# Kernel tuning notes

Hardware: AMD Instinct MI355X
Metric: run time of the kernel (lower is better)

The kernel has to match this reference:

```python
import math
import jax, jax.numpy as jnp
import numpy as np

B, T, C = 4, 2048, 1024
H = 16
HS = C // H  # head_size = 64

def setup_inputs() -> dict:
    key = jax.random.key(0)
    k1, k2, k3 = jax.random.split(key, 3)
    x = jax.random.normal(k1, (B, T, C), dtype=jnp.float32)
    W_qkv = jax.random.normal(k2, (C, 3 * C), dtype=jnp.float32) * (1.0 / math.sqrt(C))
    W_proj = jax.random.normal(k3, (C, C), dtype=jnp.float32) * (1.0 / math.sqrt(C))
    b_proj = jnp.zeros((C,), dtype=jnp.float32)
    return {"x": x, "W_qkv": W_qkv, "W_proj": W_proj, "b_proj": b_proj}

def reference(x, W_qkv, W_proj, b_proj):
    Bx, Tx, Cx = x.shape
    qkv = x @ W_qkv  # [B,T,3C]
    q, k, v = jnp.split(qkv, 3, axis=-1)
    # [B,T,C] -> [B,H,T,HS]
    def heads(t):
        return t.reshape(Bx, Tx, H, HS).transpose(0, 2, 1, 3)
    q, k, v = heads(q), heads(k), heads(v)
    scores = jnp.einsum('bhqd,bhkd->bhqk', q, k) / math.sqrt(HS)
    causal = jnp.tril(jnp.ones((Tx, Tx), dtype=bool))
    scores = jnp.where(causal, scores, -jnp.inf)
    attn = jax.nn.softmax(scores, axis=-1)
    out = jnp.einsum('bhqk,bhkd->bhqd', attn, v)  # [B,H,T,HS]
    out = out.transpose(0, 2, 1, 3).reshape(Bx, Tx, Cx)
    return out @ W_proj + b_proj
```

## Files before the change

kernel.cpp:

```cpp
#include <hip/hip_runtime.h>
#include <hip/hip_bf16.h>
#include <cstdint>
#include <cstddef>

using bf16 = __hip_bfloat16;
typedef __attribute__((ext_vector_type(8))) short short8;
typedef __attribute__((ext_vector_type(4))) float floatx4;

#define B_ 4
#define T_ 2048
#define C_ 1024
#define H_ 16
#define HS_ 64
#define BT_ (B_*T_)
#define N3C (3*C_)

#define MFMA16(a,b,c) __builtin_amdgcn_mfma_f32_16x16x32_bf16((a),(b),(c),0,0,0)

#if __has_builtin(__builtin_amdgcn_exp2f)
#define EXP2(x) __builtin_amdgcn_exp2f(x)
#else
#define EXP2(x) exp2f(x)
#endif

static __device__ __forceinline__ void gld16(const bf16* g, bf16* l) {
  __builtin_amdgcn_global_load_lds(
      (const __attribute__((address_space(1))) unsigned int*)g,
      (__attribute__((address_space(3))) unsigned int*)l, 16, 0, 0);
}

static __device__ __forceinline__ unsigned short f2bf_us(float x) {
  bf16 b = __float2bfloat16(x);
  return *(unsigned short*)&b;
}

__global__ __launch_bounds__(256)
void k_prep(const float* __restrict__ x, bf16* __restrict__ xb,
            const float* __restrict__ Wqkv, bf16* __restrict__ wqkvT,
            const float* __restrict__ Wproj, bf16* __restrict__ wprojT)
{
  const int bid = blockIdx.x, tid = threadIdx.x;
  __shared__ float tile[64][65];

  if (bid < 4096) {
    const int i = bid*256 + tid;
    const float4 v0 = ((const float4*)x)[2*i];
    const float4 v1 = ((const float4*)x)[2*i + 1];
    union { bf16 b[8]; uint4 u; } cvt;
    cvt.b[0] = __float2bfloat16(v0.x);
    cvt.b[1] = __float2bfloat16(v0.y);
    cvt.b[2] = __float2bfloat16(v0.z);
    cvt.b[3] = __float2bfloat16(v0.w);
    cvt.b[4] = __float2bfloat16(v1.x);
    cvt.b[5] = __float2bfloat16(v1.y);
    cvt.b[6] = __float2bfloat16(v1.z);
    cvt.b[7] = __float2bfloat16(v1.w);
    ((uint4*)xb)[i] = cvt.u;
    return;
  }

  const float* in; bf16* out; int N, n0, k0;
  if (bid < 4864) {
    const int j = bid - 4096;
    in = Wqkv; out = wqkvT; N = N3C;
    n0 = (j % 48) * 64; k0 = (j / 48) * 64;
  } else {
    const int j = bid - 4864;
    in = Wproj; out = wprojT; N = C_;
    n0 = (j % 16) * 64; k0 = (j / 16) * 64;
  }
  const int r = tid >> 6, c = tid & 63;
  #pragma unroll
  for (int j = 0; j < 16; ++j)
    tile[r + j*4][c] = in[(size_t)(k0 + r + j*4) * N + n0 + c];
  __syncthreads();
  #pragma unroll
  for (int j = 0; j < 16; ++j) {
    int rr = r + j*4;
    out[(size_t)(n0 + rr) * C_ + k0 + c] = __float2bfloat16(tile[c][rr]);
  }
}

template<int MODE, int NB>
__global__ __launch_bounds__(256, 2)
void k_gemm(const bf16* __restrict__ A, const bf16* __restrict__ Bt,
            int N, int K,
            bf16* __restrict__ Qb, bf16* __restrict__ Kb, bf16* __restrict__ Vt,
            float* __restrict__ Out, const float* __restrict__ bias)
{
  __shared__ __align__(16) char smem[65536];
  bf16* const sA = (bf16*)smem;
  bf16* const sB = (bf16*)(smem + 32768);

  const int tid  = threadIdx.x;
  const int lane = tid & 63, wave = tid >> 6;
  const int quad = lane >> 4, l16 = lane & 15;
  const int wm = wave >> 1, wn = wave & 1;

  const int g = blockIdx.x;
  const int xcd = g & 7;
  const int local = g >> 3;
  const int nb = local % NB;
  const int mb = (local / NB) * 8 + xcd;
  const int m0 = mb * 128, n0 = nb * 128;

  const int ra = tid >> 2;
  const int gc = (tid & 3) ^ ((ra >> 1) & 3);
  const bf16* aptr = A  + (size_t)(m0 + ra) * K + gc*8;
  const bf16* bptr = Bt + (size_t)(n0 + ra) * K + gc*8;
  const size_t rj = (size_t)64 * K;

  const int KT = K >> 5;
  floatx4 acc[4][4] = {};
  const int swz = (l16 >> 1) & 3;
  const int aoff = (wm*64 + l16)*32 + (quad ^ swz)*8;
  const int boff = (wn*64 + l16)*32 + (quad ^ swz)*8;

  #pragma unroll
  for (int t = 0; t < 3; ++t) {
    bf16* sa = sA + t*4096; bf16* sb = sB + t*4096;
    gld16(aptr + t*32,      sa + tid*8);
    gld16(aptr + rj + t*32, sa + 2048 + tid*8);
    gld16(bptr + t*32,      sb + tid*8);
    gld16(bptr + rj + t*32, sb + 2048 + tid*8);
  }

  #pragma unroll 1
  for (int i = 0; i < KT; ++i) {
    if (i < KT-2)       asm volatile("s_waitcnt vmcnt(8)" ::: "memory");
    else if (i == KT-2) asm volatile("s_waitcnt vmcnt(4)" ::: "memory");
    else                asm volatile("s_waitcnt vmcnt(0)" ::: "memory");
    asm volatile("s_barrier" ::: "memory");
    if (i < KT-3) {
      const int t = i + 3;
      bf16* sa = sA + (t & 3)*4096; bf16* sb = sB + (t & 3)*4096;
      gld16(aptr + t*32,      sa + tid*8);
      gld16(aptr + rj + t*32, sa + 2048 + tid*8);
      gld16(bptr + t*32,      sb + tid*8);
      gld16(bptr + rj + t*32, sb + 2048 + tid*8);
    }
    const bf16* sa = sA + (i & 3)*4096;
    const bf16* sb = sB + (i & 3)*4096;
    short8 af[4], bfm[4];
    #pragma unroll
    for (int ii = 0; ii < 4; ++ii) af[ii]  = *(const short8*)&sa[aoff + ii*512];
    #pragma unroll
    for (int j = 0; j < 4; ++j)    bfm[j]  = *(const short8*)&sb[boff + j*512];
    __builtin_amdgcn_s_setprio(1);
    #pragma unroll
    for (int ii = 0; ii < 4; ++ii)
      #pragma unroll
      for (int j = 0; j < 4; ++j)
        acc[ii][j] = MFMA16(af[ii], bfm[j], acc[ii][j]);
    __builtin_amdgcn_s_setprio(0);
  }

  if (MODE == 0 && nb >= 16) {
    __syncthreads();
    unsigned short* epi = (unsigned short*)smem;
    #pragma unroll
    for (int i = 0; i < 4; ++i) {
      const int tl = wm*64 + i*16 + quad*4;
      #pragma unroll
      for (int j = 0; j < 4; ++j) {
        const int ccl = wn*64 + j*16 + l16;
        #pragma unroll
        for (int r = 0; r < 4; ++r)
          epi[ccl*132 + tl + r] = f2bf_us(acc[i][j][r]);
      }
    }
    __syncthreads();
    const int b  = m0 >> 11;
    const int t0 = m0 & 2047;
    const int h0 = (n0 - 2*C_) >> 6;
    #pragma unroll
    for (int it = 0; it < 32; ++it) {
      const int id = it*256 + tid;
      const int tp = id & 31;
      const int rest = id >> 5;
      const int tl64 = (rest & 1) * 64;
      const int ccl = rest >> 1;
      const int k0p = tp + (tp & 16);
      const unsigned lo = epi[ccl*132 + tl64 + k0p];
      const unsigned hi = epi[ccl*132 + tl64 + k0p + 16];
      const int h = h0 + (ccl >> 6), d = ccl & 63;
      unsigned* row = (unsigned*)(Vt + ((size_t)(b*H_ + h) * HS_ + d) * T_);
      row[(t0 >> 1) + tl64/2 + tp] = lo | (hi << 16);
    }
  } else {
    #pragma unroll
    for (int i = 0; i < 4; ++i) {
      const int rowb = m0 + wm*64 + i*16 + quad*4;
      #pragma unroll
      for (int j = 0; j < 4; ++j) {
        const int col = n0 + wn*64 + j*16 + l16;
        #pragma unroll
        for (int r = 0; r < 4; ++r) {
          const float v = acc[i][j][r];
          const int rr = rowb + r;
          if (MODE == 0) {
            const int b = rr >> 11, t = rr & 2047;
            const int h = (col >> 6) & 15, d = col & 63;
            const size_t addr = (((size_t)(b*H_ + h) * T_ + t) << 6) + d;
            if (nb < 8) {
              Qb[addr] = __float2bfloat16(v * 0.18033688f);
            } else {
              Kb[addr] = __float2bfloat16(v);
            }
          } else {
            Out[(size_t)rr * N + col] = v + bias[col];
          }
        }
      }
    }
  }
}

__global__ __launch_bounds__(256, 3)
void k_attn(const bf16* __restrict__ Q, const bf16* __restrict__ K,
            const bf16* __restrict__ Vt, bf16* __restrict__ att)
{
  __shared__ bf16 kbuf[2][64*64];
  __shared__ bf16 vbuf[2][64*64];
  __shared__ bf16 pbuf[4][32*64];

  const int tid  = threadIdx.x;
  const int lane = tid & 63, wave = tid >> 6;
  const int quad = lane >> 4, l16 = lane & 15;
  const int x7 = l16 & 7;

  const int g  = blockIdx.x;
  const int bh = (g & 7) * 8 + ((g >> 3) & 7);
  const int qt = 15 - (g >> 6);
  const int b = bh >> 4, h = bh & 15;

  const bf16* Qp = Q  + (size_t)bh * T_ * HS_;
  const bf16* Kp = K  + (size_t)bh * T_ * HS_;
  const bf16* Vp = Vt + (size_t)bh * HS_ * T_;

  const int qbase = qt*128 + wave*32;
  const int ntk = 2*qt + 2;

  short8 qf[2][2];
  #pragma unroll
  for (int mt = 0; mt < 2; ++mt)
    #pragma unroll
    for (int ss = 0; ss < 2; ++ss)
      qf[mt][ss] = *(const short8*)(Qp + (size_t)(qbase + mt*16 + l16) * HS_ + ss*32 + quad*8);

  floatx4 o[2][4] = {};
  float lrow[2][4] = {};

  const bf16* kg[2]; const bf16* vg[2];
  int ldsoff[2];
  #pragma unroll
  for (int it = 0; it < 2; ++it) {
    const int c = it*256 + tid;
    const int row = c >> 3;
    const int col = (c & 7) ^ (row & 7);
    kg[it] = Kp + (size_t)row * HS_ + col*8;
    vg[it] = Vp + (size_t)row * T_ + col*8;
    ldsoff[it] = c*8;
  }

  bf16* pw = pbuf[wave];
  unsigned int* pw32 = (unsigned int*)pw;
  const int c0 = l16 >> 2;
  const int dwl = l16 & 3;

  for (int i = 0; i <= ntk; ++i) {
    __syncthreads();
    if (i < ntk) {
      const int stk0 = i * 64;
      bf16* kb = kbuf[i & 1];
      bf16* vb = vbuf[i & 1];
      #pragma unroll
      for (int it = 0; it < 2; ++it) {
        gld16(kg[it] + (size_t)stk0 * HS_, kb + ldsoff[it]);
        gld16(vg[it] + stk0,               vb + ldsoff[it]);
      }
    }
    if (i == 0) continue;
    const int tk  = i - 1;
    const int tk0 = tk * 64;
    if (tk0 > qbase + 31) continue;
    const bf16* kb = kbuf[tk & 1];
    const bf16* vb = vbuf[tk & 1];

    floatx4 s[2][4] = {};
    __builtin_amdgcn_s_setprio(1);
    #pragma unroll
    for (int nt = 0; nt < 4; ++nt) {
      const int key = nt*16 + l16;
      #pragma unroll
      for (int ss = 0; ss < 2; ++ss) {
        short8 kf = *(const short8*)&kb[(key*8 + ((ss*4+quad) ^ x7))*8];
        s[0][nt] = MFMA16(qf[0][ss], kf, s[0][nt]);
        s[1][nt] = MFMA16(qf[1][ss], kf, s[1][nt]);
      }
    }
    __builtin_amdgcn_s_setprio(0);

    if (tk0 + 63 > qbase) {
      #pragma unroll
      for (int mt = 0; mt < 2; ++mt)
        #pragma unroll
        for (int nt = 0; nt < 4; ++nt) {
          const int key = tk0 + nt*16 + l16;
          #pragma unroll
          for (int r = 0; r < 4; ++r) {
            const int qr = qbase + mt*16 + quad*4 + r;
            if (key > qr) s[mt][nt][r] = -1e30f;
          }
        }
    }

    #pragma unroll
    for (int mt = 0; mt < 2; ++mt) {
      #pragma unroll
      for (int r = 0; r < 4; ++r) {
        const float p0 = EXP2(s[mt][0][r]), p1 = EXP2(s[mt][1][r]);
        const float p2 = EXP2(s[mt][2][r]), p3 = EXP2(s[mt][3][r]);
        lrow[mt][r] += (p0 + p1) + (p2 + p3);
        const int q = mt*16 + quad*4 + r;
        const unsigned w0 = __builtin_amdgcn_perm(__float_as_uint(p1), __float_as_uint(p0), 0x07060302u);
        const unsigned w1 = __builtin_amdgcn_perm(__float_as_uint(p3), __float_as_uint(p2), 0x07060302u);
        pw32[q*32 + (((c0 + q)     & 7) << 2) + dwl] = w0;
        pw32[q*32 + (((c0 + q + 4) & 7) << 2) + dwl] = w1;
      }
    }

    __builtin_amdgcn_s_setprio(1);
    #pragma unroll
    for (int ss = 0; ss < 2; ++ss) {
      short8 pf0 = *(const short8*)&pw[l16*64      + ((4*ss + quad + l16) & 7)*8];
      short8 pf1 = *(const short8*)&pw[(16+l16)*64 + ((4*ss + quad + l16) & 7)*8];
      #pragma unroll
      for (int nd = 0; nd < 4; ++nd) {
        const int d = nd*16 + l16;
        short8 vf = *(const short8*)&vb[(d*8 + ((ss*4+quad) ^ x7))*8];
        o[0][nd] = MFMA16(pf0, vf, o[0][nd]);
        o[1][nd] = MFMA16(pf1, vf, o[1][nd]);
      }
    }
    __builtin_amdgcn_s_setprio(0);
  }

  #pragma unroll
  for (int mt = 0; mt < 2; ++mt) {
    #pragma unroll
    for (int r = 0; r < 4; ++r) {
      float lsum = lrow[mt][r];
      lsum += __shfl_xor(lsum, 1);
      lsum += __shfl_xor(lsum, 2);
      lsum += __shfl_xor(lsum, 4);
      lsum += __shfl_xor(lsum, 8);
      const float inv = 1.0f / lsum;
      const int tt = qbase + mt*16 + quad*4 + r;
      #pragma unroll
      for (int nd = 0; nd < 4; ++nd)
        att[(size_t)(b*T_ + tt) * C_ + h*64 + nd*16 + l16] =
            __float2bfloat16(o[mt][nd][r] * inv);
    }
  }
}

extern "C" void kernel_launch(void* const* d_in, const int* in_sizes, int n_in,
                              void* d_out, int out_size, void* d_ws, size_t ws_size,
                              hipStream_t stream) {
  const float* x     = (const float*)d_in[0];
  const float* Wqkv  = (const float*)d_in[1];
  const float* Wproj = (const float*)d_in[2];
  const float* bproj = (const float*)d_in[3];
  float* out = (float*)d_out;

  char* ws = (char*)d_ws;
  bf16* xb     = (bf16*)(ws + 0);
  bf16* wqkvT  = (bf16*)(ws + 16777216);
  bf16* wprojT = (bf16*)(ws + 23068672);
  bf16* Qb     = (bf16*)(ws + 25165824);
  bf16* Kb     = (bf16*)(ws + 41943040);
  bf16* Vt     = (bf16*)(ws + 58720256);
  bf16* att    = (bf16*)(ws + 75497472);

  k_prep<<<dim3(5120), 256, 0, stream>>>(x, xb, Wqkv, wqkvT, Wproj, wprojT);
  k_gemm<0, 24><<<dim3(1536), 256, 0, stream>>>(
      xb, wqkvT, N3C, C_, Qb, Kb, Vt, nullptr, nullptr);
  k_attn<<<dim3(1024), 256, 0, stream>>>(Qb, Kb, Vt, att);
  k_gemm<1, 8><<<dim3(512), 256, 0, stream>>>(
      att, wprojT, C_, C_, nullptr, nullptr, nullptr, out, bproj);
}
```

Before: 226.7 us.

## Use double-buffered BK=64 pipeline for QKV GEMM, keep old pipeline in projection kernel

The QKV GEMM drops its 4-stage BK=32 pipeline, which used manual vmcnt waits, in favour of a simpler double-buffered BK=64 loop. That loop uses an 8-way XOR LDS swizzle and a __syncthreads per iteration. The previous pipelined GEMM is copied into a separate k_proj kernel for the output projection, with a direct fp32 epilogue. This looks like an experiment to see whether fewer, larger k-steps beat deeper prefetch. The cost is less latency hiding, since there is only one tile in flight, plus full barriers in the QKV GEMM.

After: 225.5 us. Within noise of the previous version (-0.5%).

```diff
diff --git a/kernel.cpp b/kernel.cpp
--- a/kernel.cpp
+++ b/kernel.cpp
@@ -89,8 +89,8 @@
             float* __restrict__ Out, const float* __restrict__ bias)
 {
   __shared__ __align__(16) char smem[65536];
-  bf16* const sA = (bf16*)smem;
-  bf16* const sB = (bf16*)(smem + 32768);
+  bf16* const sAb = (bf16*)smem;
+  bf16* const sBb = (bf16*)(smem + 32768);
 
   const int tid  = threadIdx.x;
   const int lane = tid & 63, wave = tid >> 6;
@@ -104,55 +104,46 @@
   const int mb = (local / NB) * 8 + xcd;
   const int m0 = mb * 128, n0 = nb * 128;
 
-  const int ra = tid >> 2;
-  const int gc = (tid & 3) ^ ((ra >> 1) & 3);
+  const int ra = tid >> 3;
+  const int gc = (tid & 7) ^ (ra & 7);
   const bf16* aptr = A  + (size_t)(m0 + ra) * K + gc*8;
   const bf16* bptr = Bt + (size_t)(n0 + ra) * K + gc*8;
-  const size_t rj = (size_t)64 * K;
-
-  const int KT = K >> 5;
+  const size_t rj = (size_t)32 * K;
+
   floatx4 acc[4][4] = {};
-  const int swz = (l16 >> 1) & 3;
-  const int aoff = (wm*64 + l16)*32 + (quad ^ swz)*8;
-  const int boff = (wn*64 + l16)*32 + (quad ^ swz)*8;
-
-  #pragma unroll
-  for (int t = 0; t < 3; ++t) {
-    bf16* sa = sA + t*4096; bf16* sb = sB + t*4096;
-    gld16(aptr + t*32,      sa + tid*8);
-    gld16(aptr + rj + t*32, sa + 2048 + tid*8);
-    gld16(bptr + t*32,      sb + tid*8);
-    gld16(bptr + rj + t*32, sb + 2048 + tid*8);
-  }
-
-  #pragma unroll 1
-  for (int i = 0; i < KT; ++i) {
-    if (i < KT-2)       asm volatile("s_waitcnt vmcnt(8)" ::: "memory");
-    else if (i == KT-2) asm volatile("s_waitcnt vmcnt(4)" ::: "memory");
-    else                asm volatile("s_waitcnt vmcnt(0)" ::: "memory");
-    asm volatile("s_barrier" ::: "memory");
-    if (i < KT-3) {
-      const int t = i + 3;
-      bf16* sa = sA + (t & 3)*4096; bf16* sb = sB + (t & 3)*4096;
-      gld16(aptr + t*32,      sa + tid*8);
-      gld16(aptr + rj + t*32, sa + 2048 + tid*8);
-      gld16(bptr + t*32,      sb + tid*8);
-      gld16(bptr + rj + t*32, sb + 2048 + tid*8);
-    }
-    const bf16* sa = sA + (i & 3)*4096;
-    const bf16* sb = sB + (i & 3)*4096;
-    short8 af[4], bfm[4];
-    #pragma unroll
-    for (int ii = 0; ii < 4; ++ii) af[ii]  = *(const short8*)&sa[aoff + ii*512];
-    #pragma unroll
-    for (int j = 0; j < 4; ++j)    bfm[j]  = *(const short8*)&sb[boff + j*512];
-    __builtin_amdgcn_s_setprio(1);
-    #pragma unroll
-    for (int ii = 0; ii < 4; ++ii)
-      #pragma unroll
-      for (int j = 0; j < 4; ++j)
-        acc[ii][j] = MFMA16(af[ii], bfm[j], acc[ii][j]);
-    __builtin_amdgcn_s_setprio(0);
+  const int KI = K >> 6;
+  const int x7a = l16 & 7;
+
+  for (int i = 0; i <= KI; ++i) {
+    __syncthreads();
+    if (i < KI) {
+      const int k0 = i << 6;
+      bf16* sa = sAb + (i & 1) * 8192;
+      bf16* sb = sBb + (i & 1) * 8192;
+      #pragma unroll
+      for (int q2 = 0; q2 < 4; ++q2) {
+        gld16(aptr + q2*rj + k0, sa + q2*2048 + tid*8);
+        gld16(bptr + q2*rj + k0, sb + q2*2048 + tid*8);
+      }
+    }
+    if (i == 0) continue;
+    const bf16* sa = sAb + ((i-1) & 1) * 8192;
+    const bf16* sb = sBb + ((i-1) & 1) * 8192;
+    #pragma unroll
+    for (int ks = 0; ks < 2; ++ks) {
+      short8 af[4], bfm[4];
+      #pragma unroll
+      for (int ii = 0; ii < 4; ++ii)
+        af[ii] = *(const short8*)&sa[(wm*64 + ii*16 + l16)*64 + ((ks*4 + quad) ^ x7a)*8];
+      #pragma unroll
+      for (int ii = 0; ii < 4; ++ii)
+        bfm[ii] = *(const short8*)&sb[(wn*64 + ii*16 + l16)*64 + ((ks*4 + quad) ^ x7a)*8];
+      #pragma unroll
+      for (int ii = 0; ii < 4; ++ii)
+        #pragma unroll
+        for (int j = 0; j < 4; ++j)
+          acc[ii][j] = MFMA16(af[ii], bfm[j], acc[ii][j]);
+    }
   }
 
   if (MODE == 0 && nb >= 16) {
@@ -216,6 +207,91 @@
   }
 }
 
+template<int NB>
+__global__ __launch_bounds__(256, 2)
+void k_proj(const bf16* __restrict__ A, const bf16* __restrict__ Bt,
+            int N, int K, float* __restrict__ Out, const float* __restrict__ bias)
+{
+  __shared__ __align__(16) char smem[65536];
+  bf16* const sA = (bf16*)smem;
+  bf16* const sB = (bf16*)(smem + 32768);
+
+  const int tid  = threadIdx.x;
+  const int lane = tid & 63, wave = tid >> 6;
+  const int quad = lane >> 4, l16 = lane & 15;
+  const int wm = wave >> 1, wn = wave & 1;
+
+  const int g = blockIdx.x;
+  const int xcd = g & 7;
+  const int local = g >> 3;
+  const int nb = local % NB;
+  const int mb = (local / NB) * 8 + xcd;
+  const int m0 = mb * 128, n0 = nb * 128;
+
+  const int ra = tid >> 2;
+  const int gc = (tid & 3) ^ ((ra >> 1) & 3);
+  const bf16* aptr = A  + (size_t)(m0 + ra) * K + gc*8;
+  const bf16* bptr = Bt + (size_t)(n0 + ra) * K + gc*8;
+  const size_t rj = (size_t)64 * K;
+
+  const int KT = K >> 5;
+  floatx4 acc[4][4] = {};
+  const int swz = (l16 >> 1) & 3;
+  const int aoff = (wm*64 + l16)*32 + (quad ^ swz)*8;
+  const int boff = (wn*64 + l16)*32 + (quad ^ swz)*8;
+
+  #pragma unroll
+  for (int t = 0; t < 3; ++t) {
+    bf16* sa = sA + t*4096; bf16* sb = sB + t*4096;
+    gld16(aptr + t*32,      sa + tid*8);
+    gld16(aptr + rj + t*32, sa + 2048 + tid*8);
+    gld16(bptr + t*32,      sb + tid*8);
+    gld16(bptr + rj + t*32, sb + 2048 + tid*8);
+  }
+
+  #pragma unroll 1
+  for (int i = 0; i < KT; ++i) {
+    if (i < KT-2)       asm volatile("s_waitcnt vmcnt(8)" ::: "memory");
+    else if (i == KT-2) asm volatile("s_waitcnt vmcnt(4)" ::: "memory");
+    else                asm volatile("s_waitcnt vmcnt(0)" ::: "memory");
+    asm volatile("s_barrier" ::: "memory");
+    if (i < KT-3) {
+      const int t = i + 3;
+      bf16* sa = sA + (t & 3)*4096; bf16* sb = sB + (t & 3)*4096;
+      gld16(aptr + t*32,      sa + tid*8);
+      gld16(aptr + rj + t*32, sa + 2048 + tid*8);
+      gld16(bptr + t*32,      sb + tid*8);
+      gld16(bptr + rj + t*32, sb + 2048 + tid*8);
+    }
+    const bf16* sa = sA + (i & 3)*4096;
+    const bf16* sb = sB + (i & 3)*4096;
+    short8 af[4], bfm[4];
+    #pragma unroll
+    for (int ii = 0; ii < 4; ++ii) af[ii]  = *(const short8*)&sa[aoff + ii*512];
+    #pragma unroll
+    for (int j = 0; j < 4; ++j)    bfm[j]  = *(const short8*)&sb[boff + j*512];
+    __builtin_amdgcn_s_setprio(1);
+    #pragma unroll
+    for (int ii = 0; ii < 4; ++ii)
+      #pragma unroll
+      for (int j = 0; j < 4; ++j)
+        acc[ii][j] = MFMA16(af[ii], bfm[j], acc[ii][j]);
+    __builtin_amdgcn_s_setprio(0);
+  }
+
+  #pragma unroll
+  for (int i = 0; i < 4; ++i) {
+    const int rowb = m0 + wm*64 + i*16 + quad*4;
+    #pragma unroll
+    for (int j = 0; j < 4; ++j) {
+      const int col = n0 + wn*64 + j*16 + l16;
+      #pragma unroll
+      for (int r = 0; r < 4; ++r)
+        Out[(size_t)(rowb + r) * N + col] = acc[i][j][r] + bias[col];
+    }
+  }
+}
+
 __global__ __launch_bounds__(256, 3)
 void k_attn(const bf16* __restrict__ Q, const bf16* __restrict__ K,
             const bf16* __restrict__ Vt, bf16* __restrict__ att)
@@ -387,6 +463,6 @@
   k_gemm<0, 24><<<dim3(1536), 256, 0, stream>>>(
       xb, wqkvT, N3C, C_, Qb, Kb, Vt, nullptr, nullptr);
   k_attn<<<dim3(1024), 256, 0, stream>>>(Qb, Kb, Vt, att);
-  k_gemm<1, 8><<<dim3(512), 256, 0, stream>>>(
-      att, wprojT, C_, C_, nullptr, nullptr, nullptr, out, bproj);
-}
+  k_proj<8><<<dim3(512), 256, 0, stream>>>(
+      att, wprojT, C_, C_, out, bproj);
+}
```

## Add dedicated large-tile QKV GEMM kernel with 3-stage pipeline and 8 waves

Applied to the files above, without the earlier changes.

Replaces the generic QKV GEMM, which used 128x128 tiles and 1536 blocks, with a specialized kernel. Each 512-thread block computes a 256x384 tile covering matching Q, K and V column slices of one head pair, over a triple-buffered LDS pipeline that splits loads and MFMAs into half-steps with explicit barriers. The intent is more operand reuse per LDS load and better load/compute overlap. The cost is 120KB of LDS with one block per CU, only 256 blocks for the whole device, and high register pressure from 48 accumulators. The projection GEMM is split into its own simplified kernel.

Result: faster. 217.6 us (-4.0%).

```diff
diff --git a/kernel.cpp b/kernel.cpp
--- a/kernel.cpp
+++ b/kernel.cpp
@@ -81,12 +81,158 @@
   }
 }
 
-template<int MODE, int NB>
+__global__ __launch_bounds__(512, 1)
+void k_gemmqkv(const bf16* __restrict__ A, const bf16* __restrict__ Bt,
+               bf16* __restrict__ Qb, bf16* __restrict__ Kb, bf16* __restrict__ Vt)
+{
+  __shared__ __align__(16) char smem[122880];
+  bf16* const sA = (bf16*)smem;
+  bf16* const sB = (bf16*)(smem + 49152);
+
+  const int tid  = threadIdx.x;
+  const int lane = tid & 63, wave = tid >> 6;
+  const int quad = lane >> 4, l16 = lane & 15;
+  const int wm = wave >> 2, wn = wave & 3;
+
+  const int g = blockIdx.x;
+  const int xcd = g & 7;
+  const int local = g >> 3;
+  const int nb = local & 7;
+  const int mb = (local >> 3) * 8 + xcd;
+  const int m0 = mb * 256;
+  const int n0q = nb * 128;
+
+  const int ra = tid >> 2;
+  const int gc = (tid & 3) ^ ((ra >> 1) & 3);
+  const bf16* aptr = A  + (size_t)(m0 + ra) * C_ + gc*8;
+  const bf16* bp0  = Bt + (size_t)(n0q + ra) * C_ + gc*8;
+  const bf16* bp1  = Bt + (size_t)(1024 + n0q + ra) * C_ + gc*8;
+  const bf16* bp2  = Bt + (size_t)(2048 + n0q + ra) * C_ + gc*8;
+
+  floatx4 acc[8][6] = {};
+  const int swz = (l16 >> 1) & 3;
+  const int aoff = (wm*128 + l16)*32 + (quad ^ swz)*8;
+  const int boff = (wn*96  + l16)*32 + (quad ^ swz)*8;
+
+#define STAGE_A(t,s) { bf16* d = sA + (s)*8192;                     \
+    gld16(aptr + (t)*32,                  d + tid*8);               \
+    gld16(aptr + (size_t)128*C_ + (t)*32, d + 4096 + tid*8); }
+#define STAGE_B(t,s) { bf16* d = sB + (s)*12288;                    \
+    gld16(bp0 + (t)*32, d + tid*8);                                 \
+    gld16(bp1 + (t)*32, d + 4096 + tid*8);                          \
+    gld16(bp2 + (t)*32, d + 8192 + tid*8); }
+
+  STAGE_A(0,0); STAGE_B(0,0);
+  STAGE_A(1,1); STAGE_B(1,1);
+  asm volatile("s_waitcnt vmcnt(5)" ::: "memory");
+  asm volatile("s_barrier" ::: "memory");
+
+  int cs = 0;
+  #pragma unroll 1
+  for (int i = 0; i < 32; ++i) {
+    const int s2 = (cs >= 1) ? cs - 1 : 2;
+    const bf16* sa = sA + cs*8192;
+    const bf16* sb = sB + cs*12288;
+    short8 bq[6], af[4];
+    #pragma unroll
+    for (int j = 0; j < 6; ++j)    bq[j]  = *(const short8*)&sb[boff + j*512];
+    #pragma unroll
+    for (int ii = 0; ii < 4; ++ii) af[ii] = *(const short8*)&sa[aoff + ii*512];
+    if (i < 30) STAGE_A(i+2, s2);
+    asm volatile("s_barrier" ::: "memory");
+    asm volatile("s_waitcnt lgkmcnt(0)" ::: "memory");
+    __builtin_amdgcn_sched_barrier(0);
+    __builtin_amdgcn_s_setprio(1);
+    #pragma unroll
+    for (int ii = 0; ii < 4; ++ii)
+      #pragma unroll
+      for (int j = 0; j < 6; ++j)
+        acc[ii][j] = MFMA16(af[ii], bq[j], acc[ii][j]);
+    __builtin_amdgcn_s_setprio(0);
+    asm volatile("s_barrier" ::: "memory");
+    #pragma unroll
+    for (int ii = 0; ii < 4; ++ii) af[ii] = *(const short8*)&sa[aoff + (4+ii)*512];
+    if (i < 30) {
+      STAGE_B(i+2, s2);
+      asm volatile("s_waitcnt vmcnt(5)" ::: "memory");
+    } else if (i == 30) {
+      asm volatile("s_waitcnt vmcnt(0)" ::: "memory");
+    }
+    asm volatile("s_barrier" ::: "memory");
+    asm volatile("s_waitcnt lgkmcnt(0)" ::: "memory");
+    __builtin_amdgcn_sched_barrier(0);
+    __builtin_amdgcn_s_setprio(1);
+    #pragma unroll
+    for (int ii = 0; ii < 4; ++ii)
+      #pragma unroll
+      for (int j = 0; j < 6; ++j)
+        acc[4+ii][j] = MFMA16(af[ii], bq[j], acc[4+ii][j]);
+    __builtin_amdgcn_s_setprio(0);
+    asm volatile("s_barrier" ::: "memory");
+    cs = (cs == 2) ? 0 : cs + 1;
+  }
+#undef STAGE_A
+#undef STAGE_B
+
+  #pragma unroll
+  for (int ii = 0; ii < 8; ++ii) {
+    const int rowb = m0 + wm*128 + ii*16 + quad*4;
+    #pragma unroll
+    for (int j = 0; j < 6; ++j) {
+      const int L = wn*96 + j*16 + l16;
+      if (L < 256) {
+        const int gcol = (L < 128) ? (n0q + L) : (1024 + n0q + L - 128);
+        const int h = (gcol >> 6) & 15, d = gcol & 63;
+        #pragma unroll
+        for (int r = 0; r < 4; ++r) {
+          const int rr = rowb + r;
+          const int b = rr >> 11, t = rr & 2047;
+          const size_t addr = (((size_t)(b*H_ + h) * T_ + t) << 6) + d;
+          if (L < 128) Qb[addr] = __float2bfloat16(acc[ii][j][r] * 0.18033688f);
+          else         Kb[addr] = __float2bfloat16(acc[ii][j][r]);
+        }
+      }
+    }
+  }
+
+  unsigned short* epi = (unsigned short*)smem;
+  #pragma unroll
+  for (int ii = 0; ii < 8; ++ii) {
+    const int tl = wm*128 + ii*16 + quad*4;
+    #pragma unroll
+    for (int j = 0; j < 6; ++j) {
+      const int L = wn*96 + j*16 + l16;
+      if (L >= 256) {
+        const int ccl = L - 256;
+        #pragma unroll
+        for (int r = 0; r < 4; ++r)
+          epi[ccl*258 + tl + r] = f2bf_us(acc[ii][j][r]);
+      }
+    }
+  }
+  __syncthreads();
+  const int b  = m0 >> 11;
+  const int t0 = m0 & 2047;
+  #pragma unroll
+  for (int it = 0; it < 32; ++it) {
+    const int id = it*512 + tid;
+    const int tp = id & 31;
+    const int rest = id >> 5;
+    const int tl64 = (rest & 3) * 64;
+    const int ccl = rest >> 2;
+    const int k0p = tp + (tp & 16);
+    const unsigned lo = epi[ccl*258 + tl64 + k0p];
+    const unsigned hi = epi[ccl*258 + tl64 + k0p + 16];
+    const int h = nb*2 + (ccl >> 6), d = ccl & 63;
+    unsigned* row = (unsigned*)(Vt + ((size_t)(b*H_ + h) * HS_ + d) * T_);
+    row[(t0 >> 1) + tl64/2 + tp] = lo | (hi << 16);
+  }
+}
+
+template<int NB>
 __global__ __launch_bounds__(256, 2)
-void k_gemm(const bf16* __restrict__ A, const bf16* __restrict__ Bt,
-            int N, int K,
-            bf16* __restrict__ Qb, bf16* __restrict__ Kb, bf16* __restrict__ Vt,
-            float* __restrict__ Out, const float* __restrict__ bias)
+void k_proj(const bf16* __restrict__ A, const bf16* __restrict__ Bt,
+            int N, int K, float* __restrict__ Out, const float* __restrict__ bias)
 {
   __shared__ __align__(16) char smem[65536];
   bf16* const sA = (bf16*)smem;
@@ -155,63 +301,15 @@
     __builtin_amdgcn_s_setprio(0);
   }
 
-  if (MODE == 0 && nb >= 16) {
-    __syncthreads();
-    unsigned short* epi = (unsigned short*)smem;
-    #pragma unroll
-    for (int i = 0; i < 4; ++i) {
-      const int tl = wm*64 + i*16 + quad*4;
-      #pragma unroll
-      for (int j = 0; j < 4; ++j) {
-        const int ccl = wn*64 + j*16 + l16;
-        #pragma unroll
-        for (int r = 0; r < 4; ++r)
-          epi[ccl*132 + tl + r] = f2bf_us(acc[i][j][r]);
-      }
-    }
-    __syncthreads();
-    const int b  = m0 >> 11;
-    const int t0 = m0 & 2047;
-    const int h0 = (n0 - 2*C_) >> 6;
-    #pragma unroll
-    for (int it = 0; it < 32; ++it) {
-      const int id = it*256 + tid;
-      const int tp = id & 31;
-      const int rest = id >> 5;
-      const int tl64 = (rest & 1) * 64;
-      const int ccl = rest >> 1;
-      const int k0p = tp + (tp & 16);
-      const unsigned lo = epi[ccl*132 + tl64 + k0p];
-      const unsigned hi = epi[ccl*132 + tl64 + k0p + 16];
-      const int h = h0 + (ccl >> 6), d = ccl & 63;
-      unsigned* row = (unsigned*)(Vt + ((size_t)(b*H_ + h) * HS_ + d) * T_);
-      row[(t0 >> 1) + tl64/2 + tp] = lo | (hi << 16);
-    }
-  } else {
-    #pragma unroll
-    for (int i = 0; i < 4; ++i) {
-      const int rowb = m0 + wm*64 + i*16 + quad*4;
-      #pragma unroll
-      for (int j = 0; j < 4; ++j) {
-        const int col = n0 + wn*64 + j*16 + l16;
-        #pragma unroll
-        for (int r = 0; r < 4; ++r) {
-          const float v = acc[i][j][r];
-          const int rr = rowb + r;
-          if (MODE == 0) {
-            const int b = rr >> 11, t = rr & 2047;
-            const int h = (col >> 6) & 15, d = col & 63;
-            const size_t addr = (((size_t)(b*H_ + h) * T_ + t) << 6) + d;
-            if (nb < 8) {
-              Qb[addr] = __float2bfloat16(v * 0.18033688f);
-            } else {
-              Kb[addr] = __float2bfloat16(v);
-            }
-          } else {
-            Out[(size_t)rr * N + col] = v + bias[col];
-          }
-        }
-      }
+  #pragma unroll
+  for (int i = 0; i < 4; ++i) {
+    const int rowb = m0 + wm*64 + i*16 + quad*4;
+    #pragma unroll
+    for (int j = 0; j < 4; ++j) {
+      const int col = n0 + wn*64 + j*16 + l16;
+      #pragma unroll
+      for (int r = 0; r < 4; ++r)
+        Out[(size_t)(rowb + r) * N + col] = acc[i][j][r] + bias[col];
     }
   }
 }
@@ -384,9 +482,8 @@
   bf16* att    = (bf16*)(ws + 75497472);
 
   k_prep<<<dim3(5120), 256, 0, stream>>>(x, xb, Wqkv, wqkvT, Wproj, wprojT);
-  k_gemm<0, 24><<<dim3(1536), 256, 0, stream>>>(
-      xb, wqkvT, N3C, C_, Qb, Kb, Vt, nullptr, nullptr);
+  k_gemmqkv<<<dim3(256), 512, 0, stream>>>(xb, wqkvT, Qb, Kb, Vt);
   k_attn<<<dim3(1024), 256, 0, stream>>>(Qb, Kb, Vt, att);
-  k_gemm<1, 8><<<dim3(512), 256, 0, stream>>>(
-      att, wprojT, C_, C_, nullptr, nullptr, nullptr, out, bproj);
-}
+  k_proj<8><<<dim3(512), 256, 0, stream>>>(
+      att, wprojT, C_, C_, out, bproj);
+}
```
